# Optimization experiments

Measured on AMD Instinct MI355X. Metric: run time of the kernel, lower is better.

## Reference

```python
import jax, jax.numpy as jnp
import numpy as np

B, T, NQ, H = 32, 64, 128, 128


def setup_inputs() -> dict:
    key = jax.random.key(0)
    ks = jax.random.split(key, 16)
    n = lambda k, s, sc=0.05: jax.random.normal(k, s, dtype=jnp.float32) * sc
    return {
        "q": jax.random.randint(ks[0], (B, T), 0, NQ),
        "r": jax.random.randint(ks[1], (B, T), 0, 2),
        "x_emb_table": n(ks[2], (2 * NQ, H)),
        "q_emb": n(ks[3], (NQ, H)),
        "init_h": n(ks[4], (NQ, H)),
        "w1": n(ks[5], (H, 2 * H)),
        "b1": n(ks[6], (H,)),
        "w2": n(ks[7], (H, H)),
        "b2": n(ks[8], (H,)),
        "w_ih": n(ks[9], (3 * H, 2 * H)),
        "w_hh": n(ks[10], (3 * H, H)),
        "b_ih": n(ks[11], (3 * H,)),
        "b_hh": n(ks[12], (3 * H,)),
        "bias": n(ks[13], (1, NQ, 1)),
        "out_w": n(ks[14], (1, H)),
    }


def _gru_over_nodes(u, w_ih, w_hh, b_ih, b_hh):
    # Faithful to torch nn.GRU(batch_first=True) applied to [B, NQ, 2H]:
    # it recurs over the num_q axis with h0 = 0.
    h_dim = w_hh.shape[1]
    gi = jnp.einsum('bni,gi->bng', u, w_ih) + b_ih  # [B, NQ, 3H], input part precomputed

    def step(h, gi_t):  # h: [B, H], gi_t: [B, 3H]
        gh = h @ w_hh.T + b_hh
        ir, iz, inn = jnp.split(gi_t, 3, axis=-1)
        hr, hz, hn = jnp.split(gh, 3, axis=-1)
        rg = jax.nn.sigmoid(ir + hr)
        zg = jax.nn.sigmoid(iz + hz)
        ng = jnp.tanh(inn + rg * hn)
        h_new = (1.0 - zg) * ng + zg * h
        return h_new, h_new

    h0 = jnp.zeros((u.shape[0], h_dim), u.dtype)
    _, hs = jax.lax.scan(step, h0, jnp.swapaxes(gi, 0, 1))  # over NQ
    return jnp.swapaxes(hs, 0, 1)  # [B, NQ, H]


def reference(q, r, x_emb_table, q_emb, init_h, w1, b1, w2, b2,
              w_ih, w_hh, b_ih, b_hh, bias, out_w):
    bsz = q.shape[0]
    nq, hdim = q_emb.shape
    x = q + nq * r                                  # [B, T]
    x_emb = x_emb_table[x]                          # [B, T, H]
    qoh = jax.nn.one_hot(q, nq, dtype=x_emb.dtype)  # [B, T, NQ]
    ht0 = jnp.broadcast_to(init_h[None], (bsz, nq, hdim))

    def step(ht, inputs):
        xt, mask = inputs                # xt: [B,H], mask: [B,NQ]
        m3 = mask[..., None]             # [B, NQ, 1]
        # aggregate: second half is xt where qt matches, else q_emb; first half is ht either way
        other = m3 * xt[:, None, :] + (1.0 - m3) * q_emb[None]
        ht_ = jnp.concatenate([ht, other], axis=-1)          # [B, NQ, 2H]
        # update: f_neighbor is unimplemented (None->0); m = onehot * f_self(ht_)
        hs_mlp = jax.nn.relu(ht_ @ w1.T + b1) @ w2.T + b2    # mlp (eval: dropout=id)
        m = m3 * hs_mlp
        u = jnp.concatenate([m, ht], axis=-1)                # [B, NQ, 2H]
        ht_new = _gru_over_nodes(u, w_ih, w_hh, b_ih, b_hh)  # [B, NQ, H]
        yt = jax.nn.sigmoid(jnp.squeeze(ht_new @ out_w.T + bias, -1))  # [B, NQ]
        return ht_new, (ht_new, yt)

    _, (hs, ys) = jax.lax.scan(
        step, ht0, (jnp.swapaxes(x_emb, 0, 1), jnp.swapaxes(qoh, 0, 1)))
    h = jnp.concatenate([ht0[:, None], jnp.swapaxes(hs, 0, 1)], axis=1)  # [B, T+1, NQ, H]
    y = jnp.swapaxes(ys, 0, 1)                                           # [B, T, NQ]
    return y, h
```

## Files before the change

### kernel.cpp

```cpp
#include <hip/hip_runtime.h>

#define BB 32
#define TT 64
#define NQl 128
#define HD 128
#define CPAD 524
#define HPAD 132

#define NHEAT 192
#define SLOT_BYTES 8192
#define WS_FLAGS 8192
#define WS_SLOTS_OFF 16384
#define WS_NEED (WS_SLOTS_OFF + (size_t)NQl * SLOT_BYTES)

typedef _Float16 f16x8 __attribute__((ext_vector_type(8)));
typedef float f32x16 __attribute__((ext_vector_type(16)));
typedef float f32x4 __attribute__((ext_vector_type(4)));
typedef unsigned int u32x4 __attribute__((ext_vector_type(4)));
typedef int i32x4 __attribute__((ext_vector_type(4)));

__device__ __forceinline__ float sigmoidf_(float x) {
  return __builtin_amdgcn_rcpf(1.f + __expf(-x));
}
__device__ __forceinline__ float tanhf_(float x) {
  float a = fminf(fabsf(x), 15.f);
  float e = __expf(-2.f * a);
  float t = (1.f - e) * __builtin_amdgcn_rcpf(1.f + e);
  return copysignf(t, x);
}
__device__ __forceinline__ float dot4_(f32x4 a, f32x4 b) {
  return a[0] * b[0] + a[1] * b[1] + a[2] * b[2] + a[3] * b[3];
}
__device__ __forceinline__ f16x8 pack_frag_h(f32x4 a, f32x4 b) {
  f16x8 o;
  o[0] = (_Float16)a[0]; o[1] = (_Float16)a[1];
  o[2] = (_Float16)a[2]; o[3] = (_Float16)a[3];
  o[4] = (_Float16)b[0]; o[5] = (_Float16)b[1];
  o[6] = (_Float16)b[2]; o[7] = (_Float16)b[3];
  return o;
}
__device__ __forceinline__ u32x4 pack8_h(const float v[8]) {
  union { f16x8 h; u32x4 u; } c;
#pragma unroll
  for (int i = 0; i < 8; ++i) c.h[i] = (_Float16)v[i];
  return c.u;
}

__device__ __forceinline__ void issue_load32_cc(const float* p, f32x4& a, f32x4& b) {
  asm volatile(
      "global_load_dwordx4 %0, %2, off sc1\n\t"
      "global_load_dwordx4 %1, %2, off offset:16 sc1"
      : "=&v"(a), "=&v"(b) : "v"(p) : "memory");
}
__device__ __forceinline__ void wait_vm0_2(f32x4& a, f32x4& b) {
  asm volatile("s_waitcnt vmcnt(0)" : "+v"(a), "+v"(b) :: "memory");
  __builtin_amdgcn_sched_barrier(0);
}
__device__ __forceinline__ void store32_cc(float* p, f32x4 a, f32x4 b) {
  asm volatile(
      "global_store_dwordx4 %0, %1, off sc1\n\t"
      "global_store_dwordx4 %0, %2, off offset:16 sc1"
      :: "v"(p), "v"(a), "v"(b) : "memory");
}
__device__ __forceinline__ void issue_load16_cc(const void* p, u32x4& a) {
  asm volatile("global_load_dwordx4 %0, %1, off sc1" : "=&v"(a) : "v"(p) : "memory");
}
__device__ __forceinline__ void wait_vm0_1(u32x4& a) {
  asm volatile("s_waitcnt vmcnt(0)" : "+v"(a) :: "memory");
  __builtin_amdgcn_sched_barrier(0);
}
__device__ __forceinline__ void store16_cc(void* p, u32x4 v) {
  asm volatile("global_store_dwordx4 %0, %1, off sc1" :: "v"(p), "v"(v) : "memory");
}
__device__ __forceinline__ void store_flag_cc(int* p, int v) {
  asm volatile("global_store_dword %0, %1, off sc1" :: "v"(p), "v"(v) : "memory");
}
__device__ __forceinline__ int load_flag_cc(const int* p) {
  int v;
  asm volatile("global_load_dword %0, %1, off sc1\n\ts_waitcnt vmcnt(0)"
               : "=&v"(v) : "v"(p) : "memory");
  return v;
}
__device__ __forceinline__ int flagline_min(const int* p) {
  i32x4 a, b;
  asm volatile(
      "global_load_dwordx4 %0, %2, off sc1\n\t"
      "global_load_dwordx4 %1, %2, off offset:16 sc1\n\t"
      "s_waitcnt vmcnt(0)"
      : "=&v"(a), "=&v"(b) : "v"(p) : "memory");
  int m0 = min(min(a[0], a[1]), min(a[2], a[3]));
  int m1 = min(min(b[0], b[1]), min(b[2], b[3]));
  return min(m0, m1);
}

#define CHAIN(NS, S0, FR, BIASV, OUTCOL)                                        \
  {                                                                             \
    f32x16 acc;                                                                 \
    _Pragma("unroll")                                                           \
    for (int i = 0; i < 16; ++i) acc[i] = (BIASV);                              \
    _Pragma("unroll")                                                           \
    for (int ks = 0; ks < (NS); ++ks) {                                         \
      unsigned int off = ((unsigned int)(((S0) + ks) * 32 + (lhi << 4))) ^ swz; \
      f16x8 av = *(const f16x8*)(smA + rowbase + off);                          \
      acc = __builtin_amdgcn_mfma_f32_32x32x16_f16(av, FR[ks], acc, 0, 0, 0);   \
    }                                                                           \
    _Pragma("unroll")                                                           \
    for (int rg = 0; rg < 16; ++rg) {                                           \
      int br = (rg & 3) + 8 * (rg >> 2) + 4 * lhi;                              \
      sC[br * CPAD + (OUTCOL)] = acc[rg];                                       \
    }                                                                           \
  }

__global__ void __launch_bounds__(512, 2) gkt_wavefront(
    const int* __restrict__ qp, const int* __restrict__ rp_,
    const float* __restrict__ x_emb, const float* __restrict__ init_h,
    const float* __restrict__ w1, const float* __restrict__ b1,
    const float* __restrict__ w2, const float* __restrict__ b2,
    const float* __restrict__ w_ih, const float* __restrict__ w_hh,
    const float* __restrict__ b_ih, const float* __restrict__ b_hh,
    const float* __restrict__ bias, const float* __restrict__ out_w,
    float* __restrict__ y_out, float* h_out, int* wsbase,
    unsigned char* slots, int fastws) {
  const int tid = threadIdx.x;

  if ((int)blockIdx.x >= TT) {
    const int* done = wsbase + 2049;
    float z0 = 1.0f + (float)tid;
    for (int it = 0; it < 12000; ++it) {
#pragma unroll
      for (int k = 0; k < 128; ++k) z0 = __builtin_fmaf(z0, 0.9999999f, 1e-9f);
      if ((it & 7) == 0) {
        if (load_flag_cc(done) != 0) break;
      }
    }
    asm volatile("" :: "v"(z0));
    return;
  }

  __shared__ __align__(16) unsigned char smA[32 * 512];
  __shared__ float sC[32 * CPAD];
  __shared__ float sHrun[32 * HPAD];
  __shared__ float sHtp[2][32 * HPAD];
  __shared__ float sXt[32 * 128];
  __shared__ float sRed[4 * HPAD];
  __shared__ float sV1[128], sV2[128];
  __shared__ float sBias[128], sOutW[128], sB1[128], sB2[128];
  __shared__ unsigned int sMask[128];
  __shared__ int sTicket;

  const int lane = tid & 63;
  const int wv = tid >> 6;
  const int l31 = lane & 31;
  const int lhi = lane >> 5;

  int* ticket = wsbase + 2048;
  if (tid == 0) sTicket = atomicAdd(ticket, 1);
  __syncthreads();
  const int t = sTicket;

  int* myFlagWord = (int*)((char*)wsbase + (size_t)t * 128) + wv;
  const int* parentLine = (const int*)((char*)wsbase + (size_t)(t - 1) * 128);

  if (tid < 128) {
    sBias[tid] = bias[tid];
    sOutW[tid] = out_w[tid];
    sB1[tid] = b1[tid];
    sB2[tid] = b2[tid];
    sMask[tid] = 0u;
  }
  for (int i = tid; i < 32 * HPAD; i += 512) sHrun[i] = 0.f;
  __syncthreads();
  if (tid < 32) {
    int qb = qp[tid * TT + t];
    atomicOr(&sMask[qb], 1u << tid);
  }

  const int b = tid >> 4;
  const int f = tid & 15;
  const unsigned int swzb = (unsigned int)((b & 7) << 4);
  const unsigned int imgOff = (unsigned int)(b * 256) + (((unsigned int)(f * 16)) ^ swzb);
  {
    int qb = qp[b * TT + t];
    int rb = rp_[b * TT + t];
    const float* src = x_emb + (size_t)(qb + NQl * rb) * HD + f * 8;
    *(f32x4*)(sXt + b * 128 + f * 8) = *(const f32x4*)src;
    *(f32x4*)(sXt + b * 128 + f * 8 + 4) = *(const f32x4*)(src + 4);
    *(u32x4*)(smA + b * 512 + ((unsigned int)(256 + f * 16) ^ swzb)) = (u32x4)(0u);
  }

  const int gcol = wv * 32 + l31;
  f16x8 Brz[16];
#pragma unroll
  for (int ks = 0; ks < 16; ++ks) {
    const float* src = (ks < 8)
        ? (w_ih + (size_t)gcol * 256 + 128 + ks * 16 + lhi * 8)
        : (w_hh + (size_t)gcol * 128 + (ks - 8) * 16 + lhi * 8);
    Brz[ks] = pack_frag_h(*(const f32x4*)src, *(const f32x4*)(src + 4));
  }
  const int ecol = (wv < 4) ? (256 + wv * 32 + l31) : (384 + (wv - 4) * 32 + l31);
  const int erow = (wv < 4) ? ecol : (ecol - 128);
  f16x8 Bex[8];
#pragma unroll
  for (int ks = 0; ks < 8; ++ks) {
    const float* src = (wv < 4)
        ? (w_ih + (size_t)erow * 256 + 128 + ks * 16 + lhi * 8)
        : (w_hh + (size_t)erow * 128 + ks * 16 + lhi * 8);
    Bex[ks] = pack_frag_h(*(const f32x4*)src, *(const f32x4*)(src + 4));
  }
  const float brz = b_ih[gcol] + b_hh[gcol];
  const float bex = (wv < 4) ? b_ih[ecol] : b_hh[erow];

  float* hstore_base = h_out + (((size_t)b * (TT + 1) + (t + 1)) * NQl) * HD + f * 8;
  const float* hload_base = h_out + (((size_t)b * (TT + 1) + t) * NQl) * HD + f * 8;

  {
    const f32x4* s4 = (const f32x4*)init_h;
    for (int i = t * 512 + tid; i < 32 * 4096; i += TT * 512) {
      int bb = i >> 12, rem = i & 4095;
      ((f32x4*)(h_out + ((size_t)bb * (TT + 1)) * NQl * HD))[rem] = s4[rem];
    }
  }

  {
    if (t > 0) {
      if (lane == 0) {
        int c = 0;
        while (flagline_min(parentLine) < 1) {
          if (++c > (1 << 17)) break;
        }
      }
      if (fastws) {
        u32x4 pv;
        issue_load16_cc(slots + imgOff, pv);
        wait_vm0_1(pv);
        *(u32x4*)(smA + b * 512 + (((unsigned int)(f * 16)) ^ swzb)) = pv;
        union { u32x4 u; _Float16 h[8]; } cc; cc.u = pv;
#pragma unroll
        for (int i = 0; i < 8; ++i) sHtp[0][b * HPAD + f * 8 + i] = (float)cc.h[i];
      } else {
        f32x4 a0, a1;
        issue_load32_cc(hload_base, a0, a1);
        wait_vm0_2(a0, a1);
        float v[8];
        *(f32x4*)&v[0] = a0; *(f32x4*)&v[4] = a1;
        *(f32x4*)(sHtp[0] + b * HPAD + f * 8) = a0;
        *(f32x4*)(sHtp[0] + b * HPAD + f * 8 + 4) = a1;
        *(u32x4*)(smA + b * 512 + (((unsigned int)(f * 16)) ^ swzb)) = pack8_h(v);
      }
    } else {
      float v[8];
      const float* src = init_h + f * 8;
      *(f32x4*)&v[0] = *(const f32x4*)src;
      *(f32x4*)&v[4] = *(const f32x4*)(src + 4);
      *(f32x4*)(sHtp[0] + b * HPAD + f * 8) = *(f32x4*)&v[0];
      *(f32x4*)(sHtp[0] + b * HPAD + f * 8 + 4) = *(f32x4*)&v[4];
      *(u32x4*)(smA + b * 512 + (((unsigned int)(f * 16)) ^ swzb)) = pack8_h(v);
    }
  }

  const int rowbase = l31 * 512;
  const unsigned int swz = (unsigned int)((l31 & 7) << 4);

  for (int n = 0; n < NQl; ++n) {
    __syncthreads();

    CHAIN(16, 0, Brz, brz, gcol)
    if (wv < 4) { CHAIN(8, 0, Bex, bex, ecol) } else { CHAIN(8, 8, Bex, bex, ecol) }
    __syncthreads();

    unsigned int mk = sMask[n];
    while (mk) {
      const int b0 = __ffs(mk) - 1;
      mk &= mk - 1;
      const float* htp_row = sHtp[n & 1] + b0 * HPAD;
      {
        const int j = tid & 127, kq = tid >> 7;
        const float* wr = w1 + (size_t)j * 256 + kq * 64;
        const float* xr = (kq < 2) ? (htp_row + kq * 64)
                                   : (sXt + b0 * 128 + (kq - 2) * 64);
        float s = 0.f;
#pragma unroll
        for (int ii = 0; ii < 16; ++ii)
          s += dot4_(*(const f32x4*)(wr + ii * 4), *(const f32x4*)(xr + ii * 4));
        sRed[kq * HPAD + j] = s;
      }
      __syncthreads();
      if (tid < 128) {
        float v = sB1[tid] + sRed[tid] + sRed[HPAD + tid] + sRed[2 * HPAD + tid] +
                  sRed[3 * HPAD + tid];
        sV1[tid] = fmaxf(v, 0.f);
      }
      __syncthreads();
      {
        const int j = tid & 127, kq = tid >> 7;
        const float* wr = w2 + (size_t)j * 128 + kq * 32;
        const float* xr = sV1 + kq * 32;
        float s = 0.f;
#pragma unroll
        for (int ii = 0; ii < 8; ++ii)
          s += dot4_(*(const f32x4*)(wr + ii * 4), *(const f32x4*)(xr + ii * 4));
        sRed[kq * HPAD + j] = s;
      }
      __syncthreads();
      if (tid < 128)
        sV2[tid] = sB2[tid] + sRed[tid] + sRed[HPAD + tid] + sRed[2 * HPAD + tid] +
                   sRed[3 * HPAD + tid];
      __syncthreads();
      if (tid < 384) {
        const float* wr = w_ih + (size_t)tid * 256;
        float s = 0.f;
#pragma unroll
        for (int ii = 0; ii < 32; ++ii)
          s += dot4_(*(const f32x4*)(wr + ii * 4), *(const f32x4*)(sV2 + ii * 4));
        sC[b0 * CPAD + tid] += s;
      }
      __syncthreads();
    }

    float yp = 0.f;
    {
      const int j0 = f * 8;
      const float* Cb = sC + b * CPAD;
      float rpre[8], zpre[8], ipre[8], hpre[8], hold[8];
      *(f32x4*)&rpre[0] = *(const f32x4*)(Cb + j0);
      *(f32x4*)&rpre[4] = *(const f32x4*)(Cb + j0 + 4);
      *(f32x4*)&zpre[0] = *(const f32x4*)(Cb + 128 + j0);
      *(f32x4*)&zpre[4] = *(const f32x4*)(Cb + 128 + j0 + 4);
      *(f32x4*)&ipre[0] = *(const f32x4*)(Cb + 256 + j0);
      *(f32x4*)&ipre[4] = *(const f32x4*)(Cb + 256 + j0 + 4);
      *(f32x4*)&hpre[0] = *(const f32x4*)(Cb + 384 + j0);
      *(f32x4*)&hpre[4] = *(const f32x4*)(Cb + 384 + j0 + 4);
      *(f32x4*)&hold[0] = *(const f32x4*)(sHrun + b * HPAD + j0);
      *(f32x4*)&hold[4] = *(const f32x4*)(sHrun + b * HPAD + j0 + 4);
      float hnew[8];
#pragma unroll
      for (int i = 0; i < 8; ++i) {
        float rg = sigmoidf_(rpre[i]);
        float zg = sigmoidf_(zpre[i]);
        float ng = tanhf_(ipre[i] + rg * hpre[i]);
        float hv = ng + zg * (hold[i] - ng);
        hnew[i] = hv;
        yp += hv * sOutW[j0 + i];
      }
      *(f32x4*)(sHrun + b * HPAD + j0) = *(f32x4*)&hnew[0];
      *(f32x4*)(sHrun + b * HPAD + j0 + 4) = *(f32x4*)&hnew[4];
      u32x4 ph = pack8_h(hnew);
      *(u32x4*)(smA + b * 512 + ((unsigned int)(256 + f * 16) ^ swzb)) = ph;
      if (fastws) {
        float* hd = hstore_base + (size_t)n * HD;
        *(f32x4*)hd = *(f32x4*)&hnew[0];
        *(f32x4*)(hd + 4) = *(f32x4*)&hnew[4];
        store16_cc(slots + (size_t)n * SLOT_BYTES + imgOff, ph);
      } else {
        store32_cc(hstore_base + (size_t)n * HD, *(f32x4*)&hnew[0], *(f32x4*)&hnew[4]);
      }
    }

    asm volatile("s_waitcnt vmcnt(0)" ::: "memory");
    if (lane == 0) store_flag_cc(myFlagWord, n + 1);

    yp += __shfl_xor(yp, 1);
    yp += __shfl_xor(yp, 2);
    yp += __shfl_xor(yp, 4);
    yp += __shfl_xor(yp, 8);
    if (f == 0) {
      float yv = sigmoidf_(yp + sBias[n]);
      y_out[((size_t)b * TT + t) * NQl + n] = yv;
    }

    const int nn = n + 1;
    if (nn < NQl) {
      if (t > 0) {
        if (lane == 0) {
          int c = 0;
          while (flagline_min(parentLine) < nn + 1) {
            if (++c > (1 << 17)) break;
          }
        }
        if (fastws) {
          u32x4 pv;
          issue_load16_cc(slots + (size_t)nn * SLOT_BYTES + imgOff, pv);
          wait_vm0_1(pv);
          *(u32x4*)(smA + b * 512 + (((unsigned int)(f * 16)) ^ swzb)) = pv;
          union { u32x4 u; _Float16 h[8]; } cc; cc.u = pv;
#pragma unroll
          for (int i = 0; i < 8; ++i) sHtp[nn & 1][b * HPAD + f * 8 + i] = (float)cc.h[i];
        } else {
          f32x4 p0, p1;
          issue_load32_cc(hload_base + (size_t)nn * HD, p0, p1);
          wait_vm0_2(p0, p1);
          float v[8];
          *(f32x4*)&v[0] = p0; *(f32x4*)&v[4] = p1;
          *(f32x4*)(sHtp[nn & 1] + b * HPAD + f * 8) = p0;
          *(f32x4*)(sHtp[nn & 1] + b * HPAD + f * 8 + 4) = p1;
          *(u32x4*)(smA + b * 512 + (((unsigned int)(f * 16)) ^ swzb)) = pack8_h(v);
        }
      } else {
        float v[8];
        const float* src = init_h + (size_t)nn * HD + f * 8;
        *(f32x4*)&v[0] = *(const f32x4*)src;
        *(f32x4*)&v[4] = *(const f32x4*)(src + 4);
        *(f32x4*)(sHtp[nn & 1] + b * HPAD + f * 8) = *(f32x4*)&v[0];
        *(f32x4*)(sHtp[nn & 1] + b * HPAD + f * 8 + 4) = *(f32x4*)&v[4];
        *(u32x4*)(smA + b * 512 + (((unsigned int)(f * 16)) ^ swzb)) = pack8_h(v);
      }
    }
  }

  if (t == TT - 1 && tid == 0) store_flag_cc(wsbase + 2049, 1);
}

extern "C" void kernel_launch(void* const* d_in, const int* in_sizes, int n_in,
                              void* d_out, int out_size, void* d_ws, size_t ws_size,
                              hipStream_t stream) {
  (void)in_sizes; (void)n_in; (void)out_size;
  const int* q = (const int*)d_in[0];
  const int* r = (const int*)d_in[1];
  const float* x_emb = (const float*)d_in[2];
  const float* init_h = (const float*)d_in[4];
  const float* w1 = (const float*)d_in[5];
  const float* b1 = (const float*)d_in[6];
  const float* w2 = (const float*)d_in[7];
  const float* b2 = (const float*)d_in[8];
  const float* w_ih = (const float*)d_in[9];
  const float* w_hh = (const float*)d_in[10];
  const float* b_ih = (const float*)d_in[11];
  const float* b_hh = (const float*)d_in[12];
  const float* bias = (const float*)d_in[13];
  const float* out_w = (const float*)d_in[14];

  float* y_out = (float*)d_out;
  float* h_out = y_out + (size_t)BB * TT * NQl;

  int* wsbase = (int*)d_ws;
  unsigned char* slots = (unsigned char*)d_ws + WS_SLOTS_OFF;
  const int fastws = (ws_size >= WS_NEED) ? 1 : 0;

  (void)hipMemsetAsync(d_ws, 0, WS_SLOTS_OFF, stream);
  gkt_wavefront<<<TT + NHEAT, 512, 0, stream>>>(q, r, x_emb, init_h, w1, b1, w2, b2,
                                                w_ih, w_hh, b_ih, b_hh, bias, out_w,
                                                y_out, h_out, wsbase, slots, fastws);
}
```

Before: 2.566 ms.

## Drop heater blocks, batch LDS loads before MFMA, use lightweight barriers

Removes the 192 extra 'heater' blocks, which spun on FMAs to keep clocks up, and launches only the 64 wavefront blocks. The two MFMA chains now preload all 16 A fragments from LDS once and share them between the gate and extra accumulators, where before each chain reloaded them. __syncthreads is replaced with an lgkmcnt-only wait plus s_barrier. The plain h_out stores move after the flag publish, so the dependent block is signalled earlier. The risks are lower clock frequency without the heaters and higher register pressure from holding 16 fragments.

```diff
diff --git a/kernel.cpp b/kernel.cpp
--- a/kernel.cpp
+++ b/kernel.cpp
@@ -7,7 +7,6 @@
 #define CPAD 524
 #define HPAD 132
 
-#define NHEAT 192
 #define SLOT_BYTES 8192
 #define WS_FLAGS 8192
 #define WS_SLOTS_OFF 16384
@@ -46,6 +45,12 @@
   return c.u;
 }
 
+__device__ __forceinline__ void bar_lds() {
+  asm volatile("s_waitcnt lgkmcnt(0)" ::: "memory");
+  __builtin_amdgcn_s_barrier();
+  __builtin_amdgcn_sched_barrier(0);
+}
+
 __device__ __forceinline__ void issue_load32_cc(const float* p, f32x4& a, f32x4& b) {
   asm volatile(
       "global_load_dwordx4 %0, %2, off sc1\n\t"
@@ -74,12 +79,6 @@
 }
 __device__ __forceinline__ void store_flag_cc(int* p, int v) {
   asm volatile("global_store_dword %0, %1, off sc1" :: "v"(p), "v"(v) : "memory");
-}
-__device__ __forceinline__ int load_flag_cc(const int* p) {
-  int v;
-  asm volatile("global_load_dword %0, %1, off sc1\n\ts_waitcnt vmcnt(0)"
-               : "=&v"(v) : "v"(p) : "memory");
-  return v;
 }
 __device__ __forceinline__ int flagline_min(const int* p) {
   i32x4 a, b;
@@ -93,24 +92,6 @@
   return min(m0, m1);
 }
 
-#define CHAIN(NS, S0, FR, BIASV, OUTCOL)                                        \
-  {                                                                             \
-    f32x16 acc;                                                                 \
-    _Pragma("unroll")                                                           \
-    for (int i = 0; i < 16; ++i) acc[i] = (BIASV);                              \
-    _Pragma("unroll")                                                           \
-    for (int ks = 0; ks < (NS); ++ks) {                                         \
-      unsigned int off = ((unsigned int)(((S0) + ks) * 32 + (lhi << 4))) ^ swz; \
-      f16x8 av = *(const f16x8*)(smA + rowbase + off);                          \
-      acc = __builtin_amdgcn_mfma_f32_32x32x16_f16(av, FR[ks], acc, 0, 0, 0);   \
-    }                                                                           \
-    _Pragma("unroll")                                                           \
-    for (int rg = 0; rg < 16; ++rg) {                                           \
-      int br = (rg & 3) + 8 * (rg >> 2) + 4 * lhi;                              \
-      sC[br * CPAD + (OUTCOL)] = acc[rg];                                       \
-    }                                                                           \
-  }
-
 __global__ void __launch_bounds__(512, 2) gkt_wavefront(
     const int* __restrict__ qp, const int* __restrict__ rp_,
     const float* __restrict__ x_emb, const float* __restrict__ init_h,
@@ -121,22 +102,6 @@
     const float* __restrict__ bias, const float* __restrict__ out_w,
     float* __restrict__ y_out, float* h_out, int* wsbase,
     unsigned char* slots, int fastws) {
-  const int tid = threadIdx.x;
-
-  if ((int)blockIdx.x >= TT) {
-    const int* done = wsbase + 2049;
-    float z0 = 1.0f + (float)tid;
-    for (int it = 0; it < 12000; ++it) {
-#pragma unroll
-      for (int k = 0; k < 128; ++k) z0 = __builtin_fmaf(z0, 0.9999999f, 1e-9f);
-      if ((it & 7) == 0) {
-        if (load_flag_cc(done) != 0) break;
-      }
-    }
-    asm volatile("" :: "v"(z0));
-    return;
-  }
-
   __shared__ __align__(16) unsigned char smA[32 * 512];
   __shared__ float sC[32 * CPAD];
   __shared__ float sHrun[32 * HPAD];
@@ -148,6 +113,7 @@
   __shared__ unsigned int sMask[128];
   __shared__ int sTicket;
 
+  const int tid = threadIdx.x;
   const int lane = tid & 63;
   const int wv = tid >> 6;
   const int l31 = lane & 31;
@@ -262,11 +228,36 @@
   const unsigned int swz = (unsigned int)((l31 & 7) << 4);
 
   for (int n = 0; n < NQl; ++n) {
-    __syncthreads();
-
-    CHAIN(16, 0, Brz, brz, gcol)
-    if (wv < 4) { CHAIN(8, 0, Bex, bex, ecol) } else { CHAIN(8, 8, Bex, bex, ecol) }
-    __syncthreads();
+    bar_lds();
+
+    f16x8 av[16];
+#pragma unroll
+    for (int ks = 0; ks < 16; ++ks) {
+      unsigned int off = ((unsigned int)(ks * 32 + (lhi << 4))) ^ swz;
+      av[ks] = *(const f16x8*)(smA + rowbase + off);
+    }
+    f32x16 accR, accE;
+#pragma unroll
+    for (int i = 0; i < 16; ++i) { accR[i] = brz; accE[i] = bex; }
+#pragma unroll
+    for (int ks = 0; ks < 16; ++ks)
+      accR = __builtin_amdgcn_mfma_f32_32x32x16_f16(av[ks], Brz[ks], accR, 0, 0, 0);
+    if (wv < 4) {
+#pragma unroll
+      for (int ks = 0; ks < 8; ++ks)
+        accE = __builtin_amdgcn_mfma_f32_32x32x16_f16(av[ks], Bex[ks], accE, 0, 0, 0);
+    } else {
+#pragma unroll
+      for (int ks = 0; ks < 8; ++ks)
+        accE = __builtin_amdgcn_mfma_f32_32x32x16_f16(av[8 + ks], Bex[ks], accE, 0, 0, 0);
+    }
+#pragma unroll
+    for (int rg = 0; rg < 16; ++rg) {
+      int br = (rg & 3) + 8 * (rg >> 2) + 4 * lhi;
+      sC[br * CPAD + gcol] = accR[rg];
+      sC[br * CPAD + ecol] = accE[rg];
+    }
+    bar_lds();
 
     unsigned int mk = sMask[n];
     while (mk) {
@@ -284,13 +275,13 @@
           s += dot4_(*(const f32x4*)(wr + ii * 4), *(const f32x4*)(xr + ii * 4));
         sRed[kq * HPAD + j] = s;
       }
-      __syncthreads();
+      bar_lds();
       if (tid < 128) {
         float v = sB1[tid] + sRed[tid] + sRed[HPAD + tid] + sRed[2 * HPAD + tid] +
                   sRed[3 * HPAD + tid];
         sV1[tid] = fmaxf(v, 0.f);
       }
-      __syncthreads();
+      bar_lds();
       {
         const int j = tid & 127, kq = tid >> 7;
         const float* wr = w2 + (size_t)j * 128 + kq * 32;
@@ -301,11 +292,11 @@
           s += dot4_(*(const f32x4*)(wr + ii * 4), *(const f32x4*)(xr + ii * 4));
         sRed[kq * HPAD + j] = s;
       }
-      __syncthreads();
+      bar_lds();
       if (tid < 128)
         sV2[tid] = sB2[tid] + sRed[tid] + sRed[HPAD + tid] + sRed[2 * HPAD + tid] +
                    sRed[3 * HPAD + tid];
-      __syncthreads();
+      bar_lds();
       if (tid < 384) {
         const float* wr = w_ih + (size_t)tid * 256;
         float s = 0.f;
@@ -314,10 +305,11 @@
           s += dot4_(*(const f32x4*)(wr + ii * 4), *(const f32x4*)(sV2 + ii * 4));
         sC[b0 * CPAD + tid] += s;
       }
-      __syncthreads();
+      bar_lds();
     }
 
     float yp = 0.f;
+    float hnew[8];
     {
       const int j0 = f * 8;
       const float* Cb = sC + b * CPAD;
@@ -332,7 +324,6 @@
       *(f32x4*)&hpre[4] = *(const f32x4*)(Cb + 384 + j0 + 4);
       *(f32x4*)&hold[0] = *(const f32x4*)(sHrun + b * HPAD + j0);
       *(f32x4*)&hold[4] = *(const f32x4*)(sHrun + b * HPAD + j0 + 4);
-      float hnew[8];
 #pragma unroll
       for (int i = 0; i < 8; ++i) {
         float rg = sigmoidf_(rpre[i]);
@@ -347,9 +338,6 @@
       u32x4 ph = pack8_h(hnew);
       *(u32x4*)(smA + b * 512 + ((unsigned int)(256 + f * 16) ^ swzb)) = ph;
       if (fastws) {
-        float* hd = hstore_base + (size_t)n * HD;
-        *(f32x4*)hd = *(f32x4*)&hnew[0];
-        *(f32x4*)(hd + 4) = *(f32x4*)&hnew[4];
         store16_cc(slots + (size_t)n * SLOT_BYTES + imgOff, ph);
       } else {
         store32_cc(hstore_base + (size_t)n * HD, *(f32x4*)&hnew[0], *(f32x4*)&hnew[4]);
@@ -359,6 +347,11 @@
     asm volatile("s_waitcnt vmcnt(0)" ::: "memory");
     if (lane == 0) store_flag_cc(myFlagWord, n + 1);
 
+    if (fastws) {
+      float* hd = hstore_base + (size_t)n * HD;
+      *(f32x4*)hd = *(const f32x4*)&hnew[0];
+      *(f32x4*)(hd + 4) = *(const f32x4*)&hnew[4];
+    }
     yp += __shfl_xor(yp, 1);
     yp += __shfl_xor(yp, 2);
     yp += __shfl_xor(yp, 4);
@@ -406,8 +399,6 @@
       }
     }
   }
-
-  if (t == TT - 1 && tid == 0) store_flag_cc(wsbase + 2049, 1);
 }
 
 extern "C" void kernel_launch(void* const* d_in, const int* in_sizes, int n_in,
@@ -437,7 +428,7 @@
   const int fastws = (ws_size >= WS_NEED) ? 1 : 0;
 
   (void)hipMemsetAsync(d_ws, 0, WS_SLOTS_OFF, stream);
-  gkt_wavefront<<<TT + NHEAT, 512, 0, stream>>>(q, r, x_emb, init_h, w1, b1, w2, b2,
-                                                w_ih, w_hh, b_ih, b_hh, bias, out_w,
-                                                y_out, h_out, wsbase, slots, fastws);
-}
+  gkt_wavefront<<<TT, 512, 0, stream>>>(q, r, x_emb, init_h, w1, b1, w2, b2,
+                                        w_ih, w_hh, b_ih, b_hh, bias, out_w,
+                                        y_out, h_out, wsbase, slots, fastws);
+}
```

After: 2.274 ms (median of 2 runs). 11.4% less time.
